# Performance work log

Hardware: AMD Instinct MI355X
Metric: run time of the kernel (lower is better)

Reference implementation:

```python
import jax, jax.numpy as jnp
import numpy as np

THRESHOLD = 0.9
EPS = 1e-12  # F.normalize eps


def setup_inputs() -> dict:
    key = jax.random.key(0)
    clusters = jax.random.normal(key, (64, 256, 768), dtype=jnp.float32)
    return {"clusters": clusters}


def _collapse(clusters, threshold):
    B, Q, D = clusters.shape
    # F.normalize(clusters, dim=-1): divide by L2 norm clamped to eps
    norm = jnp.maximum(jnp.linalg.norm(clusters, axis=-1, keepdims=True), EPS)
    nc = clusters / norm
    sim = jnp.einsum('bqd,bkd->bqk', nc, nc)              # [B, Q, Q]
    # torch loop condition: collapse_mask[:, i, j].any() -> any over batch
    pair_flag = jnp.any(sim > threshold, axis=0)          # [Q, Q] bool, fixed before merging

    # loop order: i outer, j inner (j > i) == row-major upper triangle
    ii, jj = jnp.triu_indices(Q, k=1)
    flags = pair_flag[ii, jj]                              # [Q*(Q-1)/2]

    def step(c, x):
        i, j, f = x
        ci = jnp.take(c, i, axis=1)                        # [B, D]
        cj = jnp.take(c, j, axis=1)
        new_i = jnp.where(f, (ci + cj) * 0.5, ci)
        c = c.at[:, i].set(new_i)
        c = c.at[:, j].set(jnp.where(f, new_i, cj))        # clusters[:, j] = clusters[:, i]
        return c, None

    out, _ = jax.lax.scan(step, clusters, (ii, jj, flags))
    return out


def reference(clusters):
    return _collapse(clusters, THRESHOLD)
```

## Files before the change

### kernel.cpp

```cpp
#include <hip/hip_runtime.h>
#include <math.h>

#define BB 64
#define QQ 256
#define DD 768
#define THR 0.9f
#define EPSN 1e-12f

#define OFF_FBITS  0
#define OFF_COUNT  8192
#define OFF_PAIRS  8320
#define OFF_M      138880

using f32x4 = __attribute__((ext_vector_type(4))) float;
using s16x8 = __attribute__((ext_vector_type(8))) short;

struct Frag { float4 lo, hi; };

#define GL2LDS(g, l) __builtin_amdgcn_global_load_lds( \
    (const __attribute__((address_space(1))) void*)(g), \
    (__attribute__((address_space(3))) void*)(l), 16, 0, 0)

#define SCHED_FENCE() __builtin_amdgcn_sched_barrier(0)

__device__ __forceinline__ s16x8 cvt(const Frag& f) {
    union { s16x8 s; unsigned u[4]; } r;
    r.u[0] = __builtin_amdgcn_perm(__float_as_uint(f.lo.y), __float_as_uint(f.lo.x), 0x07060302u);
    r.u[1] = __builtin_amdgcn_perm(__float_as_uint(f.lo.w), __float_as_uint(f.lo.z), 0x07060302u);
    r.u[2] = __builtin_amdgcn_perm(__float_as_uint(f.hi.y), __float_as_uint(f.hi.x), 0x07060302u);
    r.u[3] = __builtin_amdgcn_perm(__float_as_uint(f.hi.w), __float_as_uint(f.hi.z), 0x07060302u);
    return r.s;
}
__device__ __forceinline__ float sq8(const Frag& f) {
    return f.lo.x*f.lo.x + f.lo.y*f.lo.y + f.lo.z*f.lo.z + f.lo.w*f.lo.w
         + f.hi.x*f.hi.x + f.hi.y*f.hi.y + f.hi.z*f.hi.z + f.hi.w*f.hi.w;
}

__global__ __launch_bounds__(256) void zero_kernel(unsigned* __restrict__ fbits,
                                                   int* __restrict__ count,
                                                   int* __restrict__ nflag) {
    int t = threadIdx.x;
    #pragma unroll
    for (int k = 0; k < 8; ++k) fbits[t + k * 256] = 0u;
    if (t == 0) { *count = 0; *nflag = 0; }
}

__global__ __launch_bounds__(256) void flags_kernel(const float* __restrict__ in,
                                                    float* __restrict__ out,
                                                    unsigned* __restrict__ fbits,
                                                    int* __restrict__ nflag) {
    __shared__ float lds[12288];

    int orig = blockIdx.x;
    int g = (orig & 7) * 80 + (orig >> 3);
    int tp = g % 10, b = g / 10;
    int it = 0, rem = tp, rowlen = 4;
    while (rem >= rowlen) { rem -= rowlen; ++it; --rowlen; }
    int jt = it + rem;
    int i0 = it * 64, j0 = jt * 64;

    int w = threadIdx.x >> 6, lane = threadIdx.x & 63;
    int wr = w >> 1, wc = w & 1;
    int r  = lane & 15, kg = lane >> 4;

    const float* base = in + (size_t)b * QQ * DD;

    int lr = lane >> 3;
    int lq = lane & 7;
    int swz = (lq ^ lr) * 4;
    const float* pA0 = base + (size_t)(i0 + w * 16 + lr) * DD + swz;
    const float* pA1 = pA0 + (size_t)8 * DD;
    const float* pB0 = base + (size_t)(j0 + w * 16 + lr) * DD + swz;
    const float* pB1 = pB0 + (size_t)8 * DD;

    f32x4 acc[2][2] = {};
    float4 ns = {0.f, 0.f, 0.f, 0.f};

    const f32x4* in4 = (const f32x4*)in;
    f32x4* out4 = (f32x4*)out;
    f32x4 cr[3];
    auto CLD = [&](int s) {
        int off = tp * 24 + s; off = off < 192 ? off : 191;
        cr[s % 3] = in4[(size_t)b * 49152 + (size_t)off * 256 + threadIdx.x];
    };
    auto CST = [&](int s) {
        int off = tp * 24 + s; off = off < 192 ? off : 191;
        __builtin_nontemporal_store(cr[s % 3],
            &out4[(size_t)b * 49152 + (size_t)off * 256 + threadIdx.x]);
    };

    auto STAGE = [&](int buf, int c) {
        int k0 = c * 32;
        float* L = lds + buf * 4096 + w * 512;
        GL2LDS(pA0 + k0, L);
        GL2LDS(pA1 + k0, L + 256);
        GL2LDS(pB0 + k0, L + 2048);
        GL2LDS(pB1 + k0, L + 2048 + 256);
    };
    auto RD = [&](const float* L, int row) {
        int qlo = (2 * kg) ^ (row & 7);
        Frag f;
        f.lo = *(const float4*)&L[row * 32 + qlo * 4];
        f.hi = *(const float4*)&L[row * 32 + (qlo ^ 1) * 4];
        return f;
    };
    auto CHUNK = [&](int buf) {
        const float* LA = lds + buf * 4096;
        const float* LB = LA + 2048;
        Frag fa0 = RD(LA, wr * 32 + r);
        Frag fa1 = RD(LA, wr * 32 + r + 16);
        Frag fb0 = RD(LB, wc * 32 + r);
        Frag fb1 = RD(LB, wc * 32 + r + 16);
        ns.x += sq8(fa0); ns.y += sq8(fa1); ns.z += sq8(fb0); ns.w += sq8(fb1);
        s16x8 a0 = cvt(fa0), a1 = cvt(fa1), b0 = cvt(fb0), b1 = cvt(fb1);
        acc[0][0] = __builtin_amdgcn_mfma_f32_16x16x32_bf16(a0, b0, acc[0][0], 0, 0, 0);
        acc[0][1] = __builtin_amdgcn_mfma_f32_16x16x32_bf16(a0, b1, acc[0][1], 0, 0, 0);
        acc[1][0] = __builtin_amdgcn_mfma_f32_16x16x32_bf16(a1, b0, acc[1][0], 0, 0, 0);
        acc[1][1] = __builtin_amdgcn_mfma_f32_16x16x32_bf16(a1, b1, acc[1][1], 0, 0, 0);
    };

    CLD(0); STAGE(0, 0);
    SCHED_FENCE();
    CLD(1); STAGE(1, 1);
    SCHED_FENCE();
    #pragma unroll
    for (int c = 0; c < 24; ++c) {
        if (c == 0)       asm volatile("s_waitcnt vmcnt(5)");
        else if (c == 1)  asm volatile("s_waitcnt vmcnt(6)");
        else if (c < 23)  asm volatile("s_waitcnt vmcnt(7)");
        else              asm volatile("s_waitcnt vmcnt(2)");
        asm volatile("s_waitcnt lgkmcnt(0)");
        SCHED_FENCE();
        __builtin_amdgcn_s_barrier();
        SCHED_FENCE();
        if (c < 22) { CLD(c + 2); STAGE((c + 2) % 3, c + 2); }
        CST(c);
        CHUNK(c % 3);
        SCHED_FENCE();
    }

    ns.x += __shfl_xor(ns.x, 16); ns.x += __shfl_xor(ns.x, 32);
    ns.y += __shfl_xor(ns.y, 16); ns.y += __shfl_xor(ns.y, 32);
    ns.z += __shfl_xor(ns.z, 16); ns.z += __shfl_xor(ns.z, 32);
    ns.w += __shfl_xor(ns.w, 16); ns.w += __shfl_xor(ns.w, 32);

    float njc0 = fmaxf(sqrtf(ns.z), EPSN);
    float njc1 = fmaxf(sqrtf(ns.w), EPSN);

    bool any = false;
    #pragma unroll
    for (int m = 0; m < 2; ++m) {
        float nsa = (m == 0) ? ns.x : ns.y;
        #pragma unroll
        for (int rr = 0; rr < 4; ++rr) {
            float ni2 = __shfl(nsa, kg * 4 + rr);
            float ni  = fmaxf(sqrtf(ni2), EPSN);
            int i = i0 + wr * 32 + m * 16 + kg * 4 + rr;
            int j = j0 + wc * 32 + r;
            if (j > i && acc[m][0][rr] > THR * ni * njc0) {
                int idx = i * QQ + j;
                atomicOr(&fbits[idx >> 5], 1u << (idx & 31)); any = true;
            }
            j += 16;
            if (j > i && acc[m][1][rr] > THR * ni * njc1) {
                int idx = i * QQ + j;
                atomicOr(&fbits[idx >> 5], 1u << (idx & 31)); any = true;
            }
        }
    }
    if (any) atomicAdd(nflag, 1);
}

__global__ __launch_bounds__(256) void compact_merge_kernel(const unsigned* __restrict__ fbits,
                                                            int* __restrict__ pairs,
                                                            int* __restrict__ count,
                                                            const int* __restrict__ nflag,
                                                            float* __restrict__ M) {
    int t = threadIdx.x;
    if (*nflag == 0) { if (t == 0) *count = 0; return; }

    const int P  = QQ * (QQ - 1) / 2;
    const int CH = (P + 255) / 256;
    int L0 = t * CH;
    int L1 = min(L0 + CH, P);

    int i = 0, cum = 0;
    while (i < QQ - 1 && cum + (QQ - 1 - i) <= L0) { cum += (QQ - 1 - i); ++i; }
    int j = i + 1 + (L0 - cum);

    auto getbit = [&](int ii, int jj) -> int {
        int idx = ii * QQ + jj;
        return (fbits[idx >> 5] >> (idx & 31)) & 1;
    };

    int cnt = 0;
    { int ii = i, jj = j;
      for (int L = L0; L < L1; ++L) {
          cnt += getbit(ii, jj);
          if (++jj == QQ) { ++ii; jj = ii + 1; }
      } }

    __shared__ int sc[256];
    sc[t] = cnt;
    __syncthreads();
    for (int off = 1; off < 256; off <<= 1) {
        int u = (t >= off) ? sc[t - off] : 0;
        __syncthreads();
        sc[t] += u;
        __syncthreads();
    }
    int bse = sc[t] - cnt;
    if (t == 255) *count = sc[255];

    { int ii = i, jj = j;
      for (int L = L0; L < L1; ++L) {
          if (getbit(ii, jj)) pairs[bse++] = (ii << 16) | jj;
          if (++jj == QQ) { ++ii; jj = ii + 1; }
      } }
    __syncthreads();

    int n = sc[255];
    for (int rr = 0; rr < QQ; ++rr) M[rr * QQ + t] = (rr == t) ? 1.f : 0.f;
    for (int s = 0; s < n; ++s) {
        int pr = pairs[s];
        int pi = pr >> 16, pj = pr & 0xffff;
        float nv = 0.5f * (M[pi * QQ + t] + M[pj * QQ + t]);
        M[pi * QQ + t] = nv;
        M[pj * QQ + t] = nv;
    }
}

__global__ __launch_bounds__(256) void applyM_kernel(const float* __restrict__ in,
                                                     const float* __restrict__ M,
                                                     float* __restrict__ out,
                                                     const int* __restrict__ count) {
    if (*count == 0) return;
    int b = blockIdx.x, qt = blockIdx.y;
    int t = threadIdx.x;
    for (int q = qt * 64; q < qt * 64 + 64; ++q) {
        float a0 = 0.f, a1 = 0.f, a2 = 0.f;
        for (int k = 0; k < QQ; ++k) {
            float m = M[q * QQ + k];
            if (m == 0.f) continue;
            const float* src = in + ((size_t)b * QQ + k) * DD;
            a0 += m * src[t];
            a1 += m * src[t + 256];
            a2 += m * src[t + 512];
        }
        float* dst = out + ((size_t)b * QQ + q) * DD;
        dst[t] = a0; dst[t + 256] = a1; dst[t + 512] = a2;
    }
}

extern "C" void kernel_launch(void* const* d_in, const int* in_sizes, int n_in,
                              void* d_out, int out_size, void* d_ws, size_t ws_size,
                              hipStream_t stream) {
    const float* in = (const float*)d_in[0];
    float* out = (float*)d_out;
    char* ws = (char*)d_ws;

    unsigned* fbits = (unsigned*)(ws + OFF_FBITS);
    int*   count = (int*)  (ws + OFF_COUNT);
    int*   nflag = (int*)  (ws + OFF_COUNT + 4);
    int*   pairs = (int*)  (ws + OFF_PAIRS);
    float* M     = (float*)(ws + OFF_M);

    zero_kernel<<<dim3(1), dim3(256), 0, stream>>>(fbits, count, nflag);
    flags_kernel<<<dim3(640), dim3(256), 0, stream>>>(in, out, fbits, nflag);
    compact_merge_kernel<<<dim3(1), dim3(256), 0, stream>>>(fbits, pairs, count, nflag, M);
    applyM_kernel<<<dim3(BB, 4), dim3(256), 0, stream>>>(in, M, out, count);
}
```

Before: 38.93 us.

## Double flags kernel block to 512 threads with split-K across wave groups

The flags kernel now runs 8 waves per block in two groups of four that take alternating K chunks of the bf16 MFMA Gram tile. Group 1 then writes its partial accumulators and norm sums through LDS, and group 0 reduces them. Each wave now stages half as many rows per chunk, and the out=in copy is spread across all 512 threads with a new slot mapping and a two-register ring. The aim is more waves in flight to hide memory latency, at the cost of an extra LDS reduction, a barrier, and the 512-thread launch-bounds limits on registers.

```diff
diff --git a/kernel.cpp b/kernel.cpp
--- a/kernel.cpp
+++ b/kernel.cpp
@@ -45,10 +45,10 @@
     if (t == 0) { *count = 0; *nflag = 0; }
 }
 
-__global__ __launch_bounds__(256) void flags_kernel(const float* __restrict__ in,
-                                                    float* __restrict__ out,
-                                                    unsigned* __restrict__ fbits,
-                                                    int* __restrict__ nflag) {
+__global__ __launch_bounds__(512, 5) void flags_kernel(const float* __restrict__ in,
+                                                       float* __restrict__ out,
+                                                       unsigned* __restrict__ fbits,
+                                                       int* __restrict__ nflag) {
     __shared__ float lds[12288];
 
     int orig = blockIdx.x;
@@ -59,8 +59,10 @@
     int jt = it + rem;
     int i0 = it * 64, j0 = jt * 64;
 
-    int w = threadIdx.x >> 6, lane = threadIdx.x & 63;
-    int wr = w >> 1, wc = w & 1;
+    int tid = threadIdx.x;
+    int w = tid >> 6, lane = tid & 63;
+    int grp = w >> 2, q = w & 3;
+    int wr = q >> 1, wc = q & 1;
     int r  = lane & 15, kg = lane >> 4;
 
     const float* base = in + (size_t)b * QQ * DD;
@@ -68,34 +70,28 @@
     int lr = lane >> 3;
     int lq = lane & 7;
     int swz = (lq ^ lr) * 4;
-    const float* pA0 = base + (size_t)(i0 + w * 16 + lr) * DD + swz;
-    const float* pA1 = pA0 + (size_t)8 * DD;
-    const float* pB0 = base + (size_t)(j0 + w * 16 + lr) * DD + swz;
-    const float* pB1 = pB0 + (size_t)8 * DD;
+    const float* pA = base + (size_t)(i0 + w * 8 + lr) * DD + swz;
+    const float* pB = base + (size_t)(j0 + w * 8 + lr) * DD + swz;
 
     f32x4 acc[2][2] = {};
-    float4 ns = {0.f, 0.f, 0.f, 0.f};
+    f32x4 ns = {0.f, 0.f, 0.f, 0.f};
 
     const f32x4* in4 = (const f32x4*)in;
     f32x4* out4 = (f32x4*)out;
-    f32x4 cr[3];
-    auto CLD = [&](int s) {
-        int off = tp * 24 + s; off = off < 192 ? off : 191;
-        cr[s % 3] = in4[(size_t)b * 49152 + (size_t)off * 256 + threadIdx.x];
-    };
-    auto CST = [&](int s) {
-        int off = tp * 24 + s; off = off < 192 ? off : 191;
-        __builtin_nontemporal_store(cr[s % 3],
-            &out4[(size_t)b * 49152 + (size_t)off * 256 + threadIdx.x]);
-    };
+    f32x4 cr[2];
+    auto SLOT = [&](int s) -> size_t {
+        int idx = tp * 4916 + ((s % 10) * 512 + tid);
+        idx = idx < 49151 ? idx : 49151;
+        return (size_t)b * 49152 + idx;
+    };
+    auto CLD = [&](int s) { cr[s & 1] = in4[SLOT(s)]; };
+    auto CST = [&](int s) { __builtin_nontemporal_store(cr[s & 1], &out4[SLOT(s)]); };
 
     auto STAGE = [&](int buf, int c) {
         int k0 = c * 32;
-        float* L = lds + buf * 4096 + w * 512;
-        GL2LDS(pA0 + k0, L);
-        GL2LDS(pA1 + k0, L + 256);
-        GL2LDS(pB0 + k0, L + 2048);
-        GL2LDS(pB1 + k0, L + 2048 + 256);
+        float* L = lds + buf * 4096 + w * 256;
+        GL2LDS(pA + k0, L);
+        GL2LDS(pB + k0, L + 2048);
     };
     auto RD = [&](const float* L, int row) {
         int qlo = (2 * kg) ^ (row & 7);
@@ -119,24 +115,44 @@
         acc[1][1] = __builtin_amdgcn_mfma_f32_16x16x32_bf16(a1, b1, acc[1][1], 0, 0, 0);
     };
 
-    CLD(0); STAGE(0, 0);
+    CLD(0);
+    STAGE(0, 0);
     SCHED_FENCE();
-    CLD(1); STAGE(1, 1);
+    STAGE(1, 1);
     SCHED_FENCE();
     #pragma unroll
     for (int c = 0; c < 24; ++c) {
-        if (c == 0)       asm volatile("s_waitcnt vmcnt(5)");
-        else if (c == 1)  asm volatile("s_waitcnt vmcnt(6)");
-        else if (c < 23)  asm volatile("s_waitcnt vmcnt(7)");
-        else              asm volatile("s_waitcnt vmcnt(2)");
+        if (c == 0)       asm volatile("s_waitcnt vmcnt(2)");
+        else if (c < 23)  asm volatile("s_waitcnt vmcnt(3)");
+        else              asm volatile("s_waitcnt vmcnt(1)");
         asm volatile("s_waitcnt lgkmcnt(0)");
         SCHED_FENCE();
         __builtin_amdgcn_s_barrier();
         SCHED_FENCE();
-        if (c < 22) { CLD(c + 2); STAGE((c + 2) % 3, c + 2); }
+        if (c < 23) CLD(c + 1);
+        if (c < 22) STAGE((c + 2) % 3, c + 2);
         CST(c);
-        CHUNK(c % 3);
+        if (grp == (c & 1)) CHUNK(c % 3);
         SCHED_FENCE();
+    }
+
+    if (grp == 1) {
+        float* ex = lds + (size_t)q * 1280 + lane * 20;
+        *(f32x4*)(ex +  0) = acc[0][0];
+        *(f32x4*)(ex +  4) = acc[0][1];
+        *(f32x4*)(ex +  8) = acc[1][0];
+        *(f32x4*)(ex + 12) = acc[1][1];
+        *(f32x4*)(ex + 16) = ns;
+    }
+    __syncthreads();
+    if (grp != 0) return;
+    {
+        const float* ex = lds + (size_t)q * 1280 + lane * 20;
+        acc[0][0] += *(const f32x4*)(ex +  0);
+        acc[0][1] += *(const f32x4*)(ex +  4);
+        acc[1][0] += *(const f32x4*)(ex +  8);
+        acc[1][1] += *(const f32x4*)(ex + 12);
+        ns        += *(const f32x4*)(ex + 16);
     }
 
     ns.x += __shfl_xor(ns.x, 16); ns.x += __shfl_xor(ns.x, 32);
@@ -237,17 +253,17 @@
     if (*count == 0) return;
     int b = blockIdx.x, qt = blockIdx.y;
     int t = threadIdx.x;
-    for (int q = qt * 64; q < qt * 64 + 64; ++q) {
+    for (int qq = qt * 64; qq < qt * 64 + 64; ++qq) {
         float a0 = 0.f, a1 = 0.f, a2 = 0.f;
         for (int k = 0; k < QQ; ++k) {
-            float m = M[q * QQ + k];
+            float m = M[qq * QQ + k];
             if (m == 0.f) continue;
             const float* src = in + ((size_t)b * QQ + k) * DD;
             a0 += m * src[t];
             a1 += m * src[t + 256];
             a2 += m * src[t + 512];
         }
-        float* dst = out + ((size_t)b * QQ + q) * DD;
+        float* dst = out + ((size_t)b * QQ + qq) * DD;
         dst[t] = a0; dst[t + 256] = a1; dst[t + 512] = a2;
     }
 }
@@ -266,7 +282,7 @@
     float* M     = (float*)(ws + OFF_M);
 
     zero_kernel<<<dim3(1), dim3(256), 0, stream>>>(fbits, count, nflag);
-    flags_kernel<<<dim3(640), dim3(256), 0, stream>>>(in, out, fbits, nflag);
+    flags_kernel<<<dim3(640), dim3(512), 0, stream>>>(in, out, fbits, nflag);
     compact_merge_kernel<<<dim3(1), dim3(256), 0, stream>>>(fbits, pairs, count, nflag, M);
     applyM_kernel<<<dim3(BB, 4), dim3(256), 0, stream>>>(in, M, out, count);
 }
```

After: 89.39 us. 130% more time.
